# Optimization experiments

Hardware: AMD Instinct MI355X
Metric: run time of the kernel (lower is better)

Reference implementation:

```python
import jax, jax.numpy as jnp
import numpy as np

D_IN = 4096
D_OUT = 4096
RANK = 16
NUM_EXPERTS = 8
TOP_K = 2
SCALING = 32.0 / RANK  # lora_alpha / r = 2.0


def setup_inputs() -> dict:
    key = jax.random.key(0)
    ks = jax.random.split(key, 6)
    x = jax.random.normal(ks[0], (4, 2048, D_IN), dtype=jnp.float32)
    W_base = jax.random.normal(ks[1], (D_OUT, D_IN), dtype=jnp.float32) * (1.0 / np.sqrt(D_IN))
    b_base = jax.random.normal(ks[2], (D_OUT,), dtype=jnp.float32) * 0.01
    W_router = jax.random.normal(ks[3], (NUM_EXPERTS, D_IN), dtype=jnp.float32) * 0.01
    # kaiming-uniform-like A; B nonzero (module inits B to zero, but zero B makes outputs/grads trivial)
    A_stack = jax.random.uniform(ks[4], (NUM_EXPERTS, RANK, D_IN), dtype=jnp.float32,
                                 minval=-1.0, maxval=1.0) * (1.0 / np.sqrt(D_IN))
    B_stack = jax.random.normal(ks[5], (NUM_EXPERTS, D_OUT, RANK), dtype=jnp.float32) * 0.02
    return {"x": x, "W_base": W_base, "b_base": b_base,
            "W_router": W_router, "A_stack": A_stack, "B_stack": B_stack}


def reference(x, W_base, b_base, W_router, A_stack, B_stack):
    orig_shape = x.shape
    xf = x.reshape(-1, D_IN)                                # [N, d_in]
    # Router: softmax -> top-k -> renormalize
    logits = xf @ W_router.T                                # [N, E]
    probs = jax.nn.softmax(logits, axis=-1)
    topk_p, topk_i = jax.lax.top_k(probs, TOP_K)            # [N, K]
    topk_p = topk_p / jnp.sum(topk_p, axis=-1, keepdims=True)
    # Combine weights per expert (scatter top-k probs into [N, E])
    combine = jnp.sum(jax.nn.one_hot(topk_i, NUM_EXPERTS, dtype=xf.dtype)
                      * topk_p[..., None], axis=1)          # [N, E]
    # Low-rank expert path: x @ A_e^T, weight, then @ B_e^T, summed over experts
    h = jnp.einsum('nd,erd->ner', xf, A_stack)              # [N, E, r]
    h = h * combine[..., None]
    lora_out = jnp.einsum('ner,eor->no', h, B_stack) * SCALING  # [N, d_out]
    base_out = xf @ W_base.T + b_base                       # [N, d_out]
    out = base_out + lora_out
    return out.reshape(orig_shape[:-1] + (D_OUT,))
```

## Files before the change

### kernel.cpp

```cpp
#include <hip/hip_runtime.h>

#define D_IN   4096
#define D_OUT  4096
#define N_TOK  8192
#define RANK   16
#define NEXP   8
#define ER     128
#define SCALING 2.0f

typedef __attribute__((ext_vector_type(8))) short short8;
typedef __attribute__((ext_vector_type(4))) float f32x4;
typedef __attribute__((ext_vector_type(4))) unsigned short us4;
typedef unsigned int uint;

__device__ __forceinline__ unsigned short f2bf(float f) {
  unsigned u = __float_as_uint(f);
  u += 0x7FFFu + ((u >> 16) & 1u);
  return (unsigned short)(u >> 16);
}

__device__ __forceinline__ void gload_lds16(const void* g, void* l) {
  __builtin_amdgcn_global_load_lds(
      (const __attribute__((address_space(1))) unsigned int*)g,
      (__attribute__((address_space(3))) unsigned int*)l, 16, 0, 0);
}

__global__ void prep_kernel(const float* __restrict__ W, const float* __restrict__ A,
                            const float* __restrict__ B,
                            unsigned short* __restrict__ Wb,
                            unsigned short* __restrict__ Ab,
                            unsigned short* __restrict__ Bcb) {
  const int NW4 = (D_OUT * D_IN) / 4;
  const int NA4 = (ER * D_IN) / 4;
  const int NB4 = (D_OUT * ER) / 4;
  const int total = NW4 + NA4 + NB4;
  for (int i = blockIdx.x * blockDim.x + threadIdx.x; i < total;
       i += gridDim.x * blockDim.x) {
    if (i < NW4) {
      float4 v = ((const float4*)W)[i];
      us4 o = { f2bf(v.x), f2bf(v.y), f2bf(v.z), f2bf(v.w) };
      ((us4*)Wb)[i] = o;
    } else if (i < NW4 + NA4) {
      int j = i - NW4;
      float4 v = ((const float4*)A)[j];
      us4 o = { f2bf(v.x), f2bf(v.y), f2bf(v.z), f2bf(v.w) };
      ((us4*)Ab)[j] = o;
    } else {
      int j = i - NW4 - NA4;
      int o = j >> 5; int rem = j & 31; int e = rem >> 2; int rq = rem & 3;
      float4 v = *(const float4*)(B + (size_t)e * D_OUT * RANK + o * RANK + rq * 4);
      us4 ob = { f2bf(v.x), f2bf(v.y), f2bf(v.z), f2bf(v.w) };
      ((us4*)Bcb)[j] = ob;
    }
  }
}

__global__ __launch_bounds__(256) void router_kernel(
    const float* __restrict__ X, const float* __restrict__ Wr,
    unsigned short* __restrict__ Xb, float* __restrict__ Comb) {
  int wave = threadIdx.x >> 6, lane = threadIdx.x & 63;
  int tok0 = blockIdx.x * 16 + wave * 4;
  float acc[4][8];
#pragma unroll
  for (int t = 0; t < 4; ++t)
#pragma unroll
    for (int e = 0; e < 8; ++e) acc[t][e] = 0.f;
  const float4* X4 = (const float4*)X;
  const float4* W4 = (const float4*)Wr;
#pragma unroll 1
  for (int it = 0; it < 16; ++it) {
    int kq = it * 64 + lane;
    float4 w[8];
#pragma unroll
    for (int e = 0; e < 8; ++e) w[e] = W4[e * 1024 + kq];
#pragma unroll
    for (int t = 0; t < 4; ++t) {
      float4 xv = X4[(size_t)(tok0 + t) * 1024 + kq];
      us4 xb = { f2bf(xv.x), f2bf(xv.y), f2bf(xv.z), f2bf(xv.w) };
      ((us4*)Xb)[(size_t)(tok0 + t) * 1024 + kq] = xb;
#pragma unroll
      for (int e = 0; e < 8; ++e)
        acc[t][e] = fmaf(xv.x, w[e].x, fmaf(xv.y, w[e].y,
                     fmaf(xv.z, w[e].z, fmaf(xv.w, w[e].w, acc[t][e]))));
    }
  }
#pragma unroll
  for (int t = 0; t < 4; ++t)
#pragma unroll
    for (int e = 0; e < 8; ++e) {
      float v = acc[t][e];
      for (int off = 32; off; off >>= 1) v += __shfl_xor(v, off, 64);
      acc[t][e] = v;
    }
#pragma unroll
  for (int t = 0; t < 4; ++t) {
    float m1 = acc[t][0]; int i1 = 0;
#pragma unroll
    for (int e = 1; e < 8; ++e) if (acc[t][e] > m1) { m1 = acc[t][e]; i1 = e; }
    float m2 = -1e30f; int i2 = 0;
#pragma unroll
    for (int e = 0; e < 8; ++e)
      if (e != i1 && acc[t][e] > m2) { m2 = acc[t][e]; i2 = e; }
    float w1 = 1.f / (1.f + expf(m2 - m1));
    if (lane < 8) {
      float v = (lane == i1) ? w1 : (lane == i2) ? (1.f - w1) : 0.f;
      Comb[(size_t)(tok0 + t) * 8 + lane] = v * SCALING;
    }
  }
}

__global__ __launch_bounds__(256, 2) void h_gemm_kernel(
    const unsigned short* __restrict__ Xb, const unsigned short* __restrict__ Ab,
    const float* __restrict__ Comb, unsigned short* __restrict__ Hw) {
  __shared__ unsigned short As[32 * 32];
  __shared__ unsigned short Bs[ER * 32];
  int tid = threadIdx.x, wave = tid >> 6, lane = tid & 63;
  int row0 = blockIdx.x * 32;

  int chA = wave * 64 + lane;
  int rA = chA >> 2, kA = (chA & 3) * 8;
  const unsigned short* srcA = Xb + (size_t)(row0 + rA) * D_IN + kA;
  unsigned short* dstA = As + wave * 512;
  int chB0 = (wave * 2) * 64 + lane, chB1 = chB0 + 64;
  int rB0 = chB0 >> 2, kB0 = (chB0 & 3) * 8;
  int rB1 = chB1 >> 2, kB1 = (chB1 & 3) * 8;
  const unsigned short* srcB0 = Ab + (size_t)rB0 * D_IN + kB0;
  const unsigned short* srcB1 = Ab + (size_t)rB1 * D_IN + kB1;
  unsigned short* dstB0 = Bs + (wave * 2) * 512;
  unsigned short* dstB1 = Bs + (wave * 2 + 1) * 512;

  int wm = wave >> 1, wn = wave & 1;
  f32x4 acc[4];
#pragma unroll
  for (int ni = 0; ni < 4; ++ni) acc[ni] = (f32x4){0.f, 0.f, 0.f, 0.f};

  for (int kt = 0; kt < D_IN / 32; ++kt) {
    if (wave < 2) { gload_lds16(srcA, dstA); }
    srcA += 32;
    gload_lds16(srcB0, dstB0); srcB0 += 32;
    gload_lds16(srcB1, dstB1); srcB1 += 32;
    __syncthreads();
    short8 a = *(const short8*)&As[(wm * 16 + (lane & 15)) * 32 + (lane >> 4) * 8];
    short8 b[4];
#pragma unroll
    for (int ni = 0; ni < 4; ++ni)
      b[ni] = *(const short8*)&Bs[(wn * 64 + ni * 16 + (lane & 15)) * 32 + (lane >> 4) * 8];
#pragma unroll
    for (int ni = 0; ni < 4; ++ni)
      acc[ni] = __builtin_amdgcn_mfma_f32_16x16x32_bf16(a, b[ni], acc[ni], 0, 0, 0);
    __syncthreads();
  }
#pragma unroll
  for (int ni = 0; ni < 4; ++ni) {
    int c = wn * 64 + ni * 16 + (lane & 15);
    int e = c >> 4;
#pragma unroll
    for (int i = 0; i < 4; ++i) {
      int r = row0 + wm * 16 + (lane >> 4) * 4 + i;
      float v = acc[ni][i] * Comb[(size_t)r * 8 + e];
      Hw[(size_t)r * ER + c] = f2bf(v);
    }
  }
}

__global__ __launch_bounds__(512, 2) void main_gemm_kernel(
    const unsigned short* __restrict__ Xb, const unsigned short* __restrict__ Wb,
    const unsigned short* __restrict__ Hw, const unsigned short* __restrict__ Bcb,
    const float* __restrict__ bias, float* __restrict__ Out) {
  __shared__ unsigned short lds[4 * 16384];
  char* ldsc = (char*)lds;
  const int tid = threadIdx.x;
  const int wave = tid >> 6, lane = tid & 63;
  const int wm = wave >> 2, wn = wave & 3;
  const int ks = lane >> 4;

  int bid = blockIdx.x;
  int swz = (bid & 7) * 64 + (bid >> 3);
  int mb = swz >> 4, nb = swz & 15;
  const int row0 = mb * 256, col0 = nb * 256;

  uint offX[2], offH[2], offW[2], offC[2], dstA[2], dstB[2];
#pragma unroll
  for (int c = 0; c < 2; ++c) {
    int ch = c * 512 + tid;
    int rr = ch >> 2;
    int ss = (ch & 3) ^ ((ch >> 3) & 3);
    offX[c] = (uint)(row0 + rr) * D_IN + ss * 8;
    offH[c] = (uint)(row0 + rr) * ER + ss * 8;
    offW[c] = (uint)(col0 + rr) * D_IN + ss * 8;
    offC[c] = (uint)(col0 + rr) * ER + ss * 8;
    dstA[c] = c * 8192 + wave * 1024;
    dstB[c] = 16384 + c * 8192 + wave * 1024;
  }

  uint offA[8], offB[4];
#pragma unroll
  for (int mi = 0; mi < 8; ++mi) {
    int r = wm * 128 + mi * 16 + (lane & 15);
    offA[mi] = (uint)r * 64 + (uint)((ks ^ ((r >> 1) & 3)) * 16);
  }
#pragma unroll
  for (int ni = 0; ni < 4; ++ni) {
    int r = wn * 64 + ni * 16 + (lane & 15);
    offB[ni] = 16384u + (uint)r * 64 + (uint)((ks ^ ((r >> 1) & 3)) * 16);
  }

  auto stageA = [&](int t) {
    uint sb_ = (uint)(t & 3) * 32768u;
    const unsigned short *s0, *s1;
    if (t < 128) { s0 = Xb + offX[0] + t * 32; s1 = Xb + offX[1] + t * 32; }
    else         { s0 = Hw + offH[0] + (t - 128) * 32; s1 = Hw + offH[1] + (t - 128) * 32; }
    gload_lds16(s0, ldsc + sb_ + dstA[0]);
    gload_lds16(s1, ldsc + sb_ + dstA[1]);
  };
  auto stageB = [&](int t) {
    uint sb_ = (uint)(t & 3) * 32768u;
    const unsigned short *s0, *s1;
    if (t < 128) { s0 = Wb + offW[0] + t * 32; s1 = Wb + offW[1] + t * 32; }
    else         { s0 = Bcb + offC[0] + (t - 128) * 32; s1 = Bcb + offC[1] + (t - 128) * 32; }
    gload_lds16(s0, ldsc + sb_ + dstB[0]);
    gload_lds16(s1, ldsc + sb_ + dstB[1]);
  };

  f32x4 acc[8][4];
#pragma unroll
  for (int mi = 0; mi < 8; ++mi)
#pragma unroll
    for (int ni = 0; ni < 4; ++ni) acc[mi][ni] = (f32x4){0.f, 0.f, 0.f, 0.f};

  stageA(0); stageB(0); stageA(1); stageB(1); stageA(2); stageB(2);
  asm volatile("s_waitcnt vmcnt(8)" ::: );
  __builtin_amdgcn_s_barrier();
  __builtin_amdgcn_sched_barrier(0);

#pragma unroll 1
  for (int i4 = 0; i4 < 33; ++i4) {
#pragma unroll
    for (int j = 0; j < 4; ++j) {
      const int i = i4 * 4 + j;
      const uint sb = (uint)j * 32768u;
      const int t3 = i + 3;
      short8 a0[4], bf[4];
#pragma unroll
      for (int m = 0; m < 4; ++m) a0[m] = *(const short8*)(ldsc + sb + offA[m]);
#pragma unroll
      for (int n = 0; n < 4; ++n) bf[n] = *(const short8*)(ldsc + sb + offB[n]);
      if (t3 <= 131) stageA(t3);
      __builtin_amdgcn_sched_barrier(0);
      __builtin_amdgcn_s_barrier();
      __builtin_amdgcn_sched_barrier(0);
      __builtin_amdgcn_s_setprio(1);
#pragma unroll
      for (int m = 0; m < 4; ++m)
#pragma unroll
        for (int n = 0; n < 4; ++n)
          acc[m][n] = __builtin_amdgcn_mfma_f32_16x16x32_bf16(a0[m], bf[n], acc[m][n], 0, 0, 0);
      __builtin_amdgcn_s_setprio(0);
      __builtin_amdgcn_sched_barrier(0);
      __builtin_amdgcn_s_barrier();
      __builtin_amdgcn_sched_barrier(0);
      short8 a1[4];
#pragma unroll
      for (int m = 0; m < 4; ++m) a1[m] = *(const short8*)(ldsc + sb + offA[4 + m]);
      if (t3 <= 131) stageB(t3);
      __builtin_amdgcn_sched_barrier(0);
      __builtin_amdgcn_s_barrier();
      __builtin_amdgcn_sched_barrier(0);
      __builtin_amdgcn_s_setprio(1);
#pragma unroll
      for (int m = 0; m < 4; ++m)
#pragma unroll
        for (int n = 0; n < 4; ++n)
          acc[4 + m][n] = __builtin_amdgcn_mfma_f32_16x16x32_bf16(a1[m], bf[n], acc[4 + m][n], 0, 0, 0);
      __builtin_amdgcn_s_setprio(0);
      __builtin_amdgcn_sched_barrier(0);
      if (i <= 128)      { asm volatile("s_waitcnt vmcnt(8)" ::: ); }
      else if (i == 129) { asm volatile("s_waitcnt vmcnt(4)" ::: ); }
      else if (i == 130) { asm volatile("s_waitcnt vmcnt(0)" ::: ); }
      __builtin_amdgcn_s_barrier();
      __builtin_amdgcn_sched_barrier(0);
    }
  }

#pragma unroll
  for (int ni = 0; ni < 4; ++ni) {
    const int c = col0 + wn * 64 + ni * 16 + (lane & 15);
    const float bv = bias[c];
#pragma unroll
    for (int mi = 0; mi < 8; ++mi) {
#pragma unroll
      for (int i = 0; i < 4; ++i) {
        int r = row0 + wm * 128 + mi * 16 + ks * 4 + i;
        Out[(size_t)r * D_OUT + c] = acc[mi][ni][i] + bv;
      }
    }
  }
}

extern "C" void kernel_launch(void* const* d_in, const int* in_sizes, int n_in,
                              void* d_out, int out_size, void* d_ws, size_t ws_size,
                              hipStream_t stream) {
  const float* x        = (const float*)d_in[0];
  const float* W_base   = (const float*)d_in[1];
  const float* b_base   = (const float*)d_in[2];
  const float* W_router = (const float*)d_in[3];
  const float* A_stack  = (const float*)d_in[4];
  const float* B_stack  = (const float*)d_in[5];
  float* out = (float*)d_out;

  char* ws = (char*)d_ws;
  unsigned short* Xb  = (unsigned short*)(ws);
  unsigned short* Wb  = (unsigned short*)(ws + 67108864);
  unsigned short* Ab  = (unsigned short*)(ws + 100663296);
  unsigned short* Bcb = (unsigned short*)(ws + 101711872);
  unsigned short* Hw  = (unsigned short*)(ws + 102760448);
  float*          Comb = (float*)(ws + 104857600);

  hipLaunchKernelGGL(prep_kernel, dim3(2048), dim3(256), 0, stream,
                     W_base, A_stack, B_stack, Wb, Ab, Bcb);
  hipLaunchKernelGGL(router_kernel, dim3(512), dim3(256), 0, stream,
                     x, W_router, Xb, Comb);
  hipLaunchKernelGGL(h_gemm_kernel, dim3(256), dim3(256), 0, stream,
                     Xb, Ab, Comb, Hw);
  hipLaunchKernelGGL(main_gemm_kernel, dim3(512), dim3(512), 0, stream,
                     Xb, Wb, Hw, Bcb, b_base, out);
}
```

Before: 387.4 us.

## Concatenate LoRA factors into K dimension and pipeline the h-GEMM

X and the H intermediate now share one padded row buffer (KCAT = 4096+128), and W and the reshaped B share another, so the main GEMM streams one contiguous K range without per-stage source branching. The stage loop is rewritten as macro-unrolled tiles with fixed waitcnts. The h-GEMM is rebuilt with a 128-wide K step, a 3-stage global-to-LDS pipeline and XOR-swizzled LDS, replacing its synchronous 32-wide loop. This adds a larger row stride (possible cache/TLB effects) and higher LDS use per block in the h-GEMM.

```diff
diff --git a/kernel.cpp b/kernel.cpp
--- a/kernel.cpp
+++ b/kernel.cpp
@@ -6,6 +6,7 @@
 #define RANK   16
 #define NEXP   8
 #define ER     128
+#define KCAT   4224
 #define SCALING 2.0f
 
 typedef __attribute__((ext_vector_type(8))) short short8;
@@ -27,9 +28,8 @@
 
 __global__ void prep_kernel(const float* __restrict__ W, const float* __restrict__ A,
                             const float* __restrict__ B,
-                            unsigned short* __restrict__ Wb,
-                            unsigned short* __restrict__ Ab,
-                            unsigned short* __restrict__ Bcb) {
+                            unsigned short* __restrict__ Wcat,
+                            unsigned short* __restrict__ Ab) {
   const int NW4 = (D_OUT * D_IN) / 4;
   const int NA4 = (ER * D_IN) / 4;
   const int NB4 = (D_OUT * ER) / 4;
@@ -39,7 +39,8 @@
     if (i < NW4) {
       float4 v = ((const float4*)W)[i];
       us4 o = { f2bf(v.x), f2bf(v.y), f2bf(v.z), f2bf(v.w) };
-      ((us4*)Wb)[i] = o;
+      int row = i >> 10, kq = i & 1023;
+      ((us4*)(Wcat + (size_t)row * KCAT))[kq] = o;
     } else if (i < NW4 + NA4) {
       int j = i - NW4;
       float4 v = ((const float4*)A)[j];
@@ -50,14 +51,14 @@
       int o = j >> 5; int rem = j & 31; int e = rem >> 2; int rq = rem & 3;
       float4 v = *(const float4*)(B + (size_t)e * D_OUT * RANK + o * RANK + rq * 4);
       us4 ob = { f2bf(v.x), f2bf(v.y), f2bf(v.z), f2bf(v.w) };
-      ((us4*)Bcb)[j] = ob;
+      *(us4*)(Wcat + (size_t)o * KCAT + D_IN + e * 16 + rq * 4) = ob;
     }
   }
 }
 
 __global__ __launch_bounds__(256) void router_kernel(
     const float* __restrict__ X, const float* __restrict__ Wr,
-    unsigned short* __restrict__ Xb, float* __restrict__ Comb) {
+    unsigned short* __restrict__ Xcat, float* __restrict__ Comb) {
   int wave = threadIdx.x >> 6, lane = threadIdx.x & 63;
   int tok0 = blockIdx.x * 16 + wave * 4;
   float acc[4][8];
@@ -77,7 +78,7 @@
     for (int t = 0; t < 4; ++t) {
       float4 xv = X4[(size_t)(tok0 + t) * 1024 + kq];
       us4 xb = { f2bf(xv.x), f2bf(xv.y), f2bf(xv.z), f2bf(xv.w) };
-      ((us4*)Xb)[(size_t)(tok0 + t) * 1024 + kq] = xb;
+      ((us4*)(Xcat + (size_t)(tok0 + t) * KCAT))[kq] = xb;
 #pragma unroll
       for (int e = 0; e < 8; ++e)
         acc[t][e] = fmaf(xv.x, w[e].x, fmaf(xv.y, w[e].y,
@@ -109,63 +110,132 @@
   }
 }
 
-__global__ __launch_bounds__(256, 2) void h_gemm_kernel(
-    const unsigned short* __restrict__ Xb, const unsigned short* __restrict__ Ab,
-    const float* __restrict__ Comb, unsigned short* __restrict__ Hw) {
-  __shared__ unsigned short As[32 * 32];
-  __shared__ unsigned short Bs[ER * 32];
-  int tid = threadIdx.x, wave = tid >> 6, lane = tid & 63;
-  int row0 = blockIdx.x * 32;
-
-  int chA = wave * 64 + lane;
-  int rA = chA >> 2, kA = (chA & 3) * 8;
-  const unsigned short* srcA = Xb + (size_t)(row0 + rA) * D_IN + kA;
-  unsigned short* dstA = As + wave * 512;
-  int chB0 = (wave * 2) * 64 + lane, chB1 = chB0 + 64;
-  int rB0 = chB0 >> 2, kB0 = (chB0 & 3) * 8;
-  int rB1 = chB1 >> 2, kB1 = (chB1 & 3) * 8;
-  const unsigned short* srcB0 = Ab + (size_t)rB0 * D_IN + kB0;
-  const unsigned short* srcB1 = Ab + (size_t)rB1 * D_IN + kB1;
-  unsigned short* dstB0 = Bs + (wave * 2) * 512;
-  unsigned short* dstB1 = Bs + (wave * 2 + 1) * 512;
-
-  int wm = wave >> 1, wn = wave & 1;
+#define HSTG(S) { const uint hbase = (S) * 40960u; \
+  _Pragma("unroll") for (int c = 0; c < 2; ++c) { gload_lds16(pa[c], ldsc + hbase + da[c]); pa[c] += 128; } \
+  _Pragma("unroll") for (int c = 0; c < 8; ++c) { gload_lds16(pb[c], ldsc + hbase + db[c]); pb[c] += 128; } }
+
+#define HTILE(S, S2, DOSTG, VM) { const uint hb = (S) * 40960u; \
+  short8 af[4]; short8 bfr[4][4]; \
+  _Pragma("unroll") for (int kk = 0; kk < 4; ++kk) af[kk] = *(const short8*)(ldsc + hb + oA[kk]); \
+  _Pragma("unroll") for (int n = 0; n < 4; ++n) \
+    _Pragma("unroll") for (int kk = 0; kk < 4; ++kk) bfr[n][kk] = *(const short8*)(ldsc + hb + oB[n][kk]); \
+  if (DOSTG) HSTG(S2); \
+  __builtin_amdgcn_sched_barrier(0); __builtin_amdgcn_s_barrier(); __builtin_amdgcn_sched_barrier(0); \
+  __builtin_amdgcn_s_setprio(1); \
+  _Pragma("unroll") for (int kk = 0; kk < 4; ++kk) \
+    _Pragma("unroll") for (int n = 0; n < 4; ++n) \
+      acc[n] = __builtin_amdgcn_mfma_f32_16x16x32_bf16(af[kk], bfr[n][kk], acc[n], 0, 0, 0); \
+  __builtin_amdgcn_s_setprio(0); \
+  __builtin_amdgcn_sched_barrier(0); \
+  asm volatile("s_waitcnt vmcnt(" #VM ")" ::: ); \
+  __builtin_amdgcn_s_barrier(); __builtin_amdgcn_sched_barrier(0); }
+
+__global__ __launch_bounds__(256, 1) void h_gemm_kernel(
+    unsigned short* Xcat, const unsigned short* __restrict__ Ab,
+    const float* __restrict__ Comb) {
+  __shared__ unsigned short hlds[61440];
+  char* ldsc = (char*)hlds;
+  const int tid = threadIdx.x, wave = tid >> 6, lane = tid & 63;
+  const int wm = wave >> 1, wn = wave & 1;
+  const int row0 = blockIdx.x * 32;
+
+  const unsigned short* pa[2]; uint da[2];
+#pragma unroll
+  for (int c = 0; c < 2; ++c) {
+    int ch = c * 256 + tid, row = ch >> 4, s = ch & 15;
+    pa[c] = Xcat + (size_t)(row0 + row) * KCAT + (s ^ ((row >> 1) & 7)) * 8;
+    da[c] = (uint)ch * 16;
+  }
+  const unsigned short* pb[8]; uint db[8];
+#pragma unroll
+  for (int c = 0; c < 8; ++c) {
+    int ch = c * 256 + tid, row = ch >> 4, s = ch & 15;
+    pb[c] = Ab + (size_t)row * D_IN + (s ^ ((row >> 1) & 7)) * 8;
+    db[c] = 8192u + (uint)ch * 16;
+  }
+
+  uint oA[4], oB[4][4];
+  {
+    int rA = wm * 16 + (lane & 15);
+#pragma unroll
+    for (int kk = 0; kk < 4; ++kk) {
+      int slot = kk * 4 + (lane >> 4);
+      oA[kk] = (uint)rA * 256 + (uint)((slot ^ ((rA >> 1) & 7)) * 16);
+    }
+#pragma unroll
+    for (int n = 0; n < 4; ++n) {
+      int rB = wn * 64 + n * 16 + (lane & 15);
+#pragma unroll
+      for (int kk = 0; kk < 4; ++kk) {
+        int slot = kk * 4 + (lane >> 4);
+        oB[n][kk] = 8192u + (uint)rB * 256 + (uint)((slot ^ ((rB >> 1) & 7)) * 16);
+      }
+    }
+  }
+
   f32x4 acc[4];
 #pragma unroll
-  for (int ni = 0; ni < 4; ++ni) acc[ni] = (f32x4){0.f, 0.f, 0.f, 0.f};
-
-  for (int kt = 0; kt < D_IN / 32; ++kt) {
-    if (wave < 2) { gload_lds16(srcA, dstA); }
-    srcA += 32;
-    gload_lds16(srcB0, dstB0); srcB0 += 32;
-    gload_lds16(srcB1, dstB1); srcB1 += 32;
-    __syncthreads();
-    short8 a = *(const short8*)&As[(wm * 16 + (lane & 15)) * 32 + (lane >> 4) * 8];
-    short8 b[4];
-#pragma unroll
-    for (int ni = 0; ni < 4; ++ni)
-      b[ni] = *(const short8*)&Bs[(wn * 64 + ni * 16 + (lane & 15)) * 32 + (lane >> 4) * 8];
-#pragma unroll
-    for (int ni = 0; ni < 4; ++ni)
-      acc[ni] = __builtin_amdgcn_mfma_f32_16x16x32_bf16(a, b[ni], acc[ni], 0, 0, 0);
-    __syncthreads();
-  }
-#pragma unroll
-  for (int ni = 0; ni < 4; ++ni) {
-    int c = wn * 64 + ni * 16 + (lane & 15);
+  for (int n = 0; n < 4; ++n) acc[n] = (f32x4){0.f, 0.f, 0.f, 0.f};
+
+  HSTG(0); HSTG(1);
+  asm volatile("s_waitcnt vmcnt(10)" ::: );
+  __builtin_amdgcn_s_barrier();
+  __builtin_amdgcn_sched_barrier(0);
+
+#pragma unroll 1
+  for (int i3 = 0; i3 < 10; ++i3) {
+    HTILE(0, 2, 1, 10);
+    HTILE(1, 0, 1, 10);
+    HTILE(2, 1, 1, 10);
+  }
+  HTILE(0, 0, 0, 0);
+  HTILE(1, 0, 0, 0);
+
+#pragma unroll
+  for (int n = 0; n < 4; ++n) {
+    int c = wn * 64 + n * 16 + (lane & 15);
     int e = c >> 4;
 #pragma unroll
     for (int i = 0; i < 4; ++i) {
       int r = row0 + wm * 16 + (lane >> 4) * 4 + i;
-      float v = acc[ni][i] * Comb[(size_t)r * 8 + e];
-      Hw[(size_t)r * ER + c] = f2bf(v);
-    }
-  }
-}
+      float v = acc[n][i] * Comb[(size_t)r * 8 + e];
+      Xcat[(size_t)r * KCAT + D_IN + c] = f2bf(v);
+    }
+  }
+}
+
+#define STG_A(S) { gload_lds16(pA0, ldsc + (S) * 32768u + dA0); pA0 += 32; \
+                   gload_lds16(pA1, ldsc + (S) * 32768u + dA1); pA1 += 32; }
+#define STG_B(S) { gload_lds16(pB0, ldsc + (S) * 32768u + dB0); pB0 += 32; \
+                   gload_lds16(pB1, ldsc + (S) * 32768u + dB1); pB1 += 32; }
+
+#define MTILE(SLOT, SLOT3, DOSTG, VM) { \
+  const uint sb = (SLOT) * 32768u; \
+  short8 a0[4], bf[4], a1[4]; \
+  _Pragma("unroll") for (int m = 0; m < 4; ++m) a0[m] = *(const short8*)(ldsc + sb + offA[m]); \
+  _Pragma("unroll") for (int n = 0; n < 4; ++n) bf[n] = *(const short8*)(ldsc + sb + offB[n]); \
+  if (DOSTG) STG_A(SLOT3); \
+  __builtin_amdgcn_sched_barrier(0); __builtin_amdgcn_s_barrier(); __builtin_amdgcn_sched_barrier(0); \
+  __builtin_amdgcn_s_setprio(1); \
+  _Pragma("unroll") for (int m = 0; m < 4; ++m) \
+    _Pragma("unroll") for (int n = 0; n < 4; ++n) \
+      acc[m][n] = __builtin_amdgcn_mfma_f32_16x16x32_bf16(a0[m], bf[n], acc[m][n], 0, 0, 0); \
+  __builtin_amdgcn_s_setprio(0); \
+  __builtin_amdgcn_sched_barrier(0); __builtin_amdgcn_s_barrier(); __builtin_amdgcn_sched_barrier(0); \
+  _Pragma("unroll") for (int m = 0; m < 4; ++m) a1[m] = *(const short8*)(ldsc + sb + offA[4 + m]); \
+  if (DOSTG) STG_B(SLOT3); \
+  __builtin_amdgcn_sched_barrier(0); __builtin_amdgcn_s_barrier(); __builtin_amdgcn_sched_barrier(0); \
+  __builtin_amdgcn_s_setprio(1); \
+  _Pragma("unroll") for (int m = 0; m < 4; ++m) \
+    _Pragma("unroll") for (int n = 0; n < 4; ++n) \
+      acc[4 + m][n] = __builtin_amdgcn_mfma_f32_16x16x32_bf16(a1[m], bf[n], acc[4 + m][n], 0, 0, 0); \
+  __builtin_amdgcn_s_setprio(0); \
+  __builtin_amdgcn_sched_barrier(0); \
+  asm volatile("s_waitcnt vmcnt(" #VM ")" ::: ); \
+  __builtin_amdgcn_s_barrier(); __builtin_amdgcn_sched_barrier(0); }
 
 __global__ __launch_bounds__(512, 2) void main_gemm_kernel(
-    const unsigned short* __restrict__ Xb, const unsigned short* __restrict__ Wb,
-    const unsigned short* __restrict__ Hw, const unsigned short* __restrict__ Bcb,
+    const unsigned short* __restrict__ Xcat, const unsigned short* __restrict__ Wcat,
     const float* __restrict__ bias, float* __restrict__ Out) {
   __shared__ unsigned short lds[4 * 16384];
   char* ldsc = (char*)lds;
@@ -179,18 +249,18 @@
   int mb = swz >> 4, nb = swz & 15;
   const int row0 = mb * 256, col0 = nb * 256;
 
-  uint offX[2], offH[2], offW[2], offC[2], dstA[2], dstB[2];
-#pragma unroll
-  for (int c = 0; c < 2; ++c) {
-    int ch = c * 512 + tid;
-    int rr = ch >> 2;
-    int ss = (ch & 3) ^ ((ch >> 3) & 3);
-    offX[c] = (uint)(row0 + rr) * D_IN + ss * 8;
-    offH[c] = (uint)(row0 + rr) * ER + ss * 8;
-    offW[c] = (uint)(col0 + rr) * D_IN + ss * 8;
-    offC[c] = (uint)(col0 + rr) * ER + ss * 8;
-    dstA[c] = c * 8192 + wave * 1024;
-    dstB[c] = 16384 + c * 8192 + wave * 1024;
+  const unsigned short *pA0, *pA1, *pB0, *pB1;
+  uint dA0, dA1, dB0, dB1;
+  {
+    int ch0 = tid, ch1 = 512 + tid;
+    int rr0 = ch0 >> 2, ss0 = (ch0 & 3) ^ ((ch0 >> 3) & 3);
+    int rr1 = ch1 >> 2, ss1 = (ch1 & 3) ^ ((ch1 >> 3) & 3);
+    pA0 = Xcat + (size_t)(row0 + rr0) * KCAT + ss0 * 8;
+    pA1 = Xcat + (size_t)(row0 + rr1) * KCAT + ss1 * 8;
+    pB0 = Wcat + (size_t)(col0 + rr0) * KCAT + ss0 * 8;
+    pB1 = Wcat + (size_t)(col0 + rr1) * KCAT + ss1 * 8;
+    dA0 = (uint)wave * 1024;          dA1 = 8192u + (uint)wave * 1024;
+    dB0 = 16384u + (uint)wave * 1024; dB1 = 24576u + (uint)wave * 1024;
   }
 
   uint offA[8], offB[4];
@@ -205,82 +275,28 @@
     offB[ni] = 16384u + (uint)r * 64 + (uint)((ks ^ ((r >> 1) & 3)) * 16);
   }
 
-  auto stageA = [&](int t) {
-    uint sb_ = (uint)(t & 3) * 32768u;
-    const unsigned short *s0, *s1;
-    if (t < 128) { s0 = Xb + offX[0] + t * 32; s1 = Xb + offX[1] + t * 32; }
-    else         { s0 = Hw + offH[0] + (t - 128) * 32; s1 = Hw + offH[1] + (t - 128) * 32; }
-    gload_lds16(s0, ldsc + sb_ + dstA[0]);
-    gload_lds16(s1, ldsc + sb_ + dstA[1]);
-  };
-  auto stageB = [&](int t) {
-    uint sb_ = (uint)(t & 3) * 32768u;
-    const unsigned short *s0, *s1;
-    if (t < 128) { s0 = Wb + offW[0] + t * 32; s1 = Wb + offW[1] + t * 32; }
-    else         { s0 = Bcb + offC[0] + (t - 128) * 32; s1 = Bcb + offC[1] + (t - 128) * 32; }
-    gload_lds16(s0, ldsc + sb_ + dstB[0]);
-    gload_lds16(s1, ldsc + sb_ + dstB[1]);
-  };
-
   f32x4 acc[8][4];
 #pragma unroll
   for (int mi = 0; mi < 8; ++mi)
 #pragma unroll
     for (int ni = 0; ni < 4; ++ni) acc[mi][ni] = (f32x4){0.f, 0.f, 0.f, 0.f};
 
-  stageA(0); stageB(0); stageA(1); stageB(1); stageA(2); stageB(2);
+  STG_A(0); STG_B(0); STG_A(1); STG_B(1); STG_A(2); STG_B(2);
   asm volatile("s_waitcnt vmcnt(8)" ::: );
   __builtin_amdgcn_s_barrier();
   __builtin_amdgcn_sched_barrier(0);
 
 #pragma unroll 1
-  for (int i4 = 0; i4 < 33; ++i4) {
-#pragma unroll
-    for (int j = 0; j < 4; ++j) {
-      const int i = i4 * 4 + j;
-      const uint sb = (uint)j * 32768u;
-      const int t3 = i + 3;
-      short8 a0[4], bf[4];
-#pragma unroll
-      for (int m = 0; m < 4; ++m) a0[m] = *(const short8*)(ldsc + sb + offA[m]);
-#pragma unroll
-      for (int n = 0; n < 4; ++n) bf[n] = *(const short8*)(ldsc + sb + offB[n]);
-      if (t3 <= 131) stageA(t3);
-      __builtin_amdgcn_sched_barrier(0);
-      __builtin_amdgcn_s_barrier();
-      __builtin_amdgcn_sched_barrier(0);
-      __builtin_amdgcn_s_setprio(1);
-#pragma unroll
-      for (int m = 0; m < 4; ++m)
-#pragma unroll
-        for (int n = 0; n < 4; ++n)
-          acc[m][n] = __builtin_amdgcn_mfma_f32_16x16x32_bf16(a0[m], bf[n], acc[m][n], 0, 0, 0);
-      __builtin_amdgcn_s_setprio(0);
-      __builtin_amdgcn_sched_barrier(0);
-      __builtin_amdgcn_s_barrier();
-      __builtin_amdgcn_sched_barrier(0);
-      short8 a1[4];
-#pragma unroll
-      for (int m = 0; m < 4; ++m) a1[m] = *(const short8*)(ldsc + sb + offA[4 + m]);
-      if (t3 <= 131) stageB(t3);
-      __builtin_amdgcn_sched_barrier(0);
-      __builtin_amdgcn_s_barrier();
-      __builtin_amdgcn_sched_barrier(0);
-      __builtin_amdgcn_s_setprio(1);
-#pragma unroll
-      for (int m = 0; m < 4; ++m)
-#pragma unroll
-        for (int n = 0; n < 4; ++n)
-          acc[4 + m][n] = __builtin_amdgcn_mfma_f32_16x16x32_bf16(a1[m], bf[n], acc[4 + m][n], 0, 0, 0);
-      __builtin_amdgcn_s_setprio(0);
-      __builtin_amdgcn_sched_barrier(0);
-      if (i <= 128)      { asm volatile("s_waitcnt vmcnt(8)" ::: ); }
-      else if (i == 129) { asm volatile("s_waitcnt vmcnt(4)" ::: ); }
-      else if (i == 130) { asm volatile("s_waitcnt vmcnt(0)" ::: ); }
-      __builtin_amdgcn_s_barrier();
-      __builtin_amdgcn_sched_barrier(0);
-    }
-  }
+  for (int i4 = 0; i4 < 32; ++i4) {
+    MTILE(0, 3, 1, 8);
+    MTILE(1, 0, 1, 8);
+    MTILE(2, 1, 1, 8);
+    MTILE(3, 2, 1, 8);
+  }
+  MTILE(0, 3, 1, 8);
+  MTILE(1, 0, 0, 4);
+  MTILE(2, 0, 0, 0);
+  MTILE(3, 0, 0, 0);
 
 #pragma unroll
   for (int ni = 0; ni < 4; ++ni) {
@@ -309,19 +325,17 @@
   float* out = (float*)d_out;
 
   char* ws = (char*)d_ws;
-  unsigned short* Xb  = (unsigned short*)(ws);
-  unsigned short* Wb  = (unsigned short*)(ws + 67108864);
-  unsigned short* Ab  = (unsigned short*)(ws + 100663296);
-  unsigned short* Bcb = (unsigned short*)(ws + 101711872);
-  unsigned short* Hw  = (unsigned short*)(ws + 102760448);
+  unsigned short* Xcat = (unsigned short*)(ws);
+  unsigned short* Wcat = (unsigned short*)(ws + 69206016);
+  unsigned short* Ab   = (unsigned short*)(ws + 103809024);
   float*          Comb = (float*)(ws + 104857600);
 
   hipLaunchKernelGGL(prep_kernel, dim3(2048), dim3(256), 0, stream,
-                     W_base, A_stack, B_stack, Wb, Ab, Bcb);
+                     W_base, A_stack, B_stack, Wcat, Ab);
   hipLaunchKernelGGL(router_kernel, dim3(512), dim3(256), 0, stream,
-                     x, W_router, Xb, Comb);
+                     x, W_router, Xcat, Comb);
   hipLaunchKernelGGL(h_gemm_kernel, dim3(256), dim3(256), 0, stream,
-                     Xb, Ab, Comb, Hw);
+                     Xcat, Ab, Comb);
   hipLaunchKernelGGL(main_gemm_kernel, dim3(512), dim3(512), 0, stream,
-                     Xb, Wb, Hw, Bcb, b_base, out);
-}
+                     Xcat, Wcat, b_base, out);
+}
```

Result: faster. 335.5 us (-13.4%).
